# Kernel tuning notes

Hardware: AMD Instinct MI355X
Metric: run time of the kernel (lower is better)

The kernel has to match this reference:

```python
import jax, jax.numpy as jnp
import numpy as np
import math

S, B, H, NH = 2048, 2, 2048, 16
HN = H // NH  # head dim = 128

def setup_inputs() -> dict:
    key = jax.random.key(0)
    ks = jax.random.split(key, 5)
    hidden_states = jax.random.normal(ks[0], (S, B, H), dtype=jnp.float32)
    # causal mask: True means masked (filled with -10000), broadcast over heads
    attention_mask = jnp.triu(jnp.ones((S, S), dtype=bool), k=1)[None, None].repeat(B, axis=0)
    w_qkv = jax.random.normal(ks[1], (3 * H, H), dtype=jnp.float32) * (1.0 / math.sqrt(H))
    b_qkv = jax.random.normal(ks[2], (3 * H,), dtype=jnp.float32) * 0.02
    w_dense = jax.random.normal(ks[3], (H, H), dtype=jnp.float32) * (1.0 / math.sqrt(H))
    b_dense = jax.random.normal(ks[4], (H,), dtype=jnp.float32) * 0.02
    return {"hidden_states": hidden_states, "attention_mask": attention_mask,
            "w_qkv": w_qkv, "b_qkv": b_qkv, "w_dense": w_dense, "b_dense": b_dense}

def reference(hidden_states, attention_mask, w_qkv, b_qkv, w_dense, b_dense):
    s, b, h = hidden_states.shape
    nh, hn = NH, h // NH
    # QKV projection (ColumnParallelLinear, world_size=1)
    qkv = hidden_states @ w_qkv.T + b_qkv                # [s, b, 3h]
    qkv = qkv.reshape(s, b, nh, 3 * hn)
    q, k, v = jnp.split(qkv, 3, axis=-1)                 # each [s, b, nh, hn]
    q = q.transpose(1, 2, 0, 3)                          # [b, nh, s, hn]
    k = k.transpose(1, 2, 0, 3)
    v = v.transpose(1, 2, 0, 3)
    # norm_factor = sqrt(hn)*coeff, softmax rescales by coeff -> net 1/sqrt(hn)
    scores = jnp.einsum('bnqh,bnkh->bnqk', q, k) / jnp.float32(math.sqrt(hn))
    scores = jnp.where(attention_mask, jnp.float32(-10000.0), scores)
    probs = jax.nn.softmax(scores, axis=-1)              # [b, nh, s, s]
    ctx = jnp.einsum('bnqk,bnkh->bnqh', probs, v)        # [b, nh, s, hn]
    ctx = ctx.transpose(2, 0, 1, 3).reshape(s, b, h)     # [s, b, h]
    # RowParallelLinear with skip_bias_add=True: bias returned separately
    output = ctx @ w_dense.T
    return output, b_dense
```

## Files before the change

kernel.cpp:

```cpp
#include <hip/hip_runtime.h>

typedef unsigned short u16;
typedef unsigned int   u32;
typedef __attribute__((ext_vector_type(8))) short bf16x8;
typedef __attribute__((ext_vector_type(4))) float f32x4;

#define S_LEN 2048
#define B_SZ  2
#define H_DIM 2048
#define NH_   16
#define HN_   128
#define M_TOK 4096
#define NQKV  6144
#define NT_   (S_LEN / 64)

__device__ __forceinline__ u16 f2bf(float f) {
    u32 x = __float_as_uint(f);
    return (u16)((x + 0x7fffu + ((x >> 16) & 1u)) >> 16);
}

__device__ __forceinline__ void async16(const void* g, void* l) {
    __builtin_amdgcn_global_load_lds((const __attribute__((address_space(1))) void*)g,
                                     (__attribute__((address_space(3))) void*)l,
                                     16, 0, 0);
}

__global__ __launch_bounds__(256) void cvt3(
    const float* __restrict__ a, u16* __restrict__ oa, int na,
    const float* __restrict__ b, u16* __restrict__ ob, int nb,
    const float* __restrict__ c, u16* __restrict__ oc, int nc)
{
    int g = blockIdx.x * 256 + threadIdx.x;
    const float* in; u16* out; int idx;
    if (g < na)           { in = a; out = oa; idx = g; }
    else if (g < na + nb) { in = b; out = ob; idx = g - na; }
    else if (g < na + nb + nc) { in = c; out = oc; idx = g - na - nb; }
    else return;
    int i = idx * 4;
    float4 v = *(const float4*)&in[i];
    ushort4 o;
    o.x = f2bf(v.x); o.y = f2bf(v.y); o.z = f2bf(v.z); o.w = f2bf(v.w);
    *(ushort4*)&out[i] = o;
}

template<int EPI>
__global__ __launch_bounds__(256) void gemm_mfma(
    const u16* __restrict__ A, const u16* __restrict__ W,
    const float* __restrict__ bias, float* __restrict__ Cout,
    u16* __restrict__ Qb, u16* __restrict__ Kb, u16* __restrict__ Vt,
    int M, int N, int K)
{
    __shared__ __align__(16) u16 Af[2][8 * 64 * 8];
    __shared__ __align__(16) u16 Bf[2][8 * 64 * 8];
    const int t = threadIdx.x, l = t & 63, w = t >> 6;
    const int quad = l >> 4, ln = l & 15;
    const int wm = w >> 1, wn = w & 1;
    const int m0 = blockIdx.y * 128, n0 = blockIdx.x * 128;

    f32x4 acc[4][4];
#pragma unroll
    for (int i = 0; i < 4; ++i)
#pragma unroll
        for (int j = 0; j < 4; ++j)
#pragma unroll
            for (int r = 0; r < 4; ++r) acc[i][j][r] = 0.f;

    auto stage = [&](int buf, int k0) {
#pragma unroll
        for (int i = 0; i < 2; ++i) {
            int mb = i * 4 + w;
            async16(&A[(size_t)(m0 + mb * 16 + ln) * K + k0 + quad * 8],
                    &Af[buf][(mb * 64 + l) * 8]);
            async16(&W[(size_t)(n0 + mb * 16 + ln) * K + k0 + quad * 8],
                    &Bf[buf][(mb * 64 + l) * 8]);
        }
    };

    stage(0, 0);
    __syncthreads();

    const int NIT = K / 32;
#pragma unroll 1
    for (int kk = 0; kk < NIT; ++kk) {
        const int cur = kk & 1;
        if (kk + 1 < NIT) stage(cur ^ 1, (kk + 1) * 32);

        bf16x8 af[4], bfr[4];
#pragma unroll
        for (int x = 0; x < 4; ++x) {
            af[x]  = *(const bf16x8*)&Af[cur][((wm * 4 + x) * 64 + l) * 8];
            bfr[x] = *(const bf16x8*)&Bf[cur][((wn * 4 + x) * 64 + l) * 8];
        }
#pragma unroll
        for (int mt = 0; mt < 4; ++mt)
#pragma unroll
            for (int nt = 0; nt < 4; ++nt)
                acc[mt][nt] = __builtin_amdgcn_mfma_f32_16x16x32_bf16(
                    af[mt], bfr[nt], acc[mt][nt], 0, 0, 0);
        __syncthreads();
    }

    if constexpr (EPI == 0) {
#pragma unroll
        for (int mt = 0; mt < 4; ++mt)
#pragma unroll
            for (int nt = 0; nt < 4; ++nt) {
                int col = n0 + (wn * 4 + nt) * 16 + ln;
#pragma unroll
                for (int r = 0; r < 4; ++r) {
                    int row = m0 + wm * 64 + mt * 16 + quad * 4 + r;
                    Cout[(size_t)row * N + col] = acc[mt][nt][r];
                }
            }
    } else {
        const float kQS = 0.08838834764831845f * 1.44269504088896340f;
#pragma unroll
        for (int nt = 0; nt < 4; ++nt) {
            int col  = n0 + (wn * 4 + nt) * 16 + ln;
            int head = col / 384;
            int g    = col - head * 384;
            int sec  = g >> 7;
            int d    = g & 127;
            float bv = bias[col];
#pragma unroll
            for (int mt = 0; mt < 4; ++mt)
#pragma unroll
                for (int r = 0; r < 4; ++r) {
                    int tok = m0 + wm * 64 + mt * 16 + quad * 4 + r;
                    int s = tok >> 1, bb = tok & 1;
                    float v = acc[mt][nt][r] + bv;
                    if (sec == 0)
                        Qb[((size_t)(bb * NH_ + head) * S_LEN + s) * HN_ + d] = f2bf(v * kQS);
                    else if (sec == 1)
                        Kb[((size_t)(bb * NH_ + head) * S_LEN + s) * HN_ + d] = f2bf(v);
                    else
                        Vt[((size_t)(bb * NH_ + head) * HN_ + d) * S_LEN + s] = f2bf(v);
                }
        }
    }
}

__global__ __launch_bounds__(256) void attn_mfma(
    const u16* __restrict__ Qb, const u16* __restrict__ Kb,
    const u16* __restrict__ Vt, u16* __restrict__ Ctx)
{
    __shared__ __align__(16) u16 Ks[2][16 * 64 * 8];
    __shared__ __align__(16) u16 Vs[2][16 * 64 * 8];
    __shared__ __align__(16) u16 Psm[4][16][72];

    const int t = threadIdx.x, l = t & 63, w = t >> 6;
    const int quad = l >> 4, ln = l & 15;
    const int j = blockIdx.x;
    const int n = blockIdx.y, b = blockIdx.z;
    const u16* Qh = Qb + (size_t)(b * NH_ + n) * S_LEN * HN_;
    const u16* Kh = Kb + (size_t)(b * NH_ + n) * S_LEN * HN_;
    const u16* Vh = Vt + (size_t)(b * NH_ + n) * HN_ * S_LEN;

#pragma unroll 1
    for (int phase = 0; phase < 2; ++phase) {
        const int qt = phase ? j : (NT_ - 1 - j);
        const int q0 = qt * 64;

#pragma unroll
        for (int i = 0; i < 4; ++i)
            async16(&Qh[(size_t)(q0 + i * 16 + ln) * HN_ + w * 32 + quad * 8],
                    &Ks[1][((i * 4 + w) * 64 + l) * 8]);
#pragma unroll
        for (int i = 0; i < 4; ++i) {
            async16(&Kh[(size_t)(i * 16 + ln) * HN_ + w * 32 + quad * 8],
                    &Ks[0][((i * 4 + w) * 64 + l) * 8]);
            int dv = i * 4 + w, dt = dv >> 1, ks = dv & 1;
            async16(&Vh[(size_t)(dt * 16 + ln) * S_LEN + ks * 32 + quad * 8],
                    &Vs[0][(dv * 64 + l) * 8]);
        }
        __syncthreads();

        bf16x8 qf[4];
#pragma unroll
        for (int ks = 0; ks < 4; ++ks)
            qf[ks] = *(const bf16x8*)&Ks[1][((w * 4 + ks) * 64 + l) * 8];
        __syncthreads();

        float m_i[4], l_i[4];
        f32x4 acco[8];
#pragma unroll
        for (int r = 0; r < 4; ++r) { m_i[r] = -1e30f; l_i[r] = 0.f; }
#pragma unroll
        for (int dt = 0; dt < 8; ++dt)
#pragma unroll
            for (int r = 0; r < 4; ++r) acco[dt][r] = 0.f;

#pragma unroll 1
        for (int kt = 0; kt <= qt; ++kt) {
            const int cur = kt & 1;

            if (kt < qt) {
                const int nxt = cur ^ 1;
#pragma unroll
                for (int i = 0; i < 4; ++i) {
                    async16(&Kh[(size_t)((kt + 1) * 64 + i * 16 + ln) * HN_ + w * 32 + quad * 8],
                            &Ks[nxt][((i * 4 + w) * 64 + l) * 8]);
                    int dv = i * 4 + w, dt = dv >> 1, ks = dv & 1;
                    async16(&Vh[(size_t)(dt * 16 + ln) * S_LEN + (kt + 1) * 64 + ks * 32 + quad * 8],
                            &Vs[nxt][(dv * 64 + l) * 8]);
                }
            }

            f32x4 sc[4];
#pragma unroll
            for (int nt = 0; nt < 4; ++nt)
#pragma unroll
                for (int r = 0; r < 4; ++r) sc[nt][r] = 0.f;
#pragma unroll
            for (int nt = 0; nt < 4; ++nt)
#pragma unroll
                for (int ks = 0; ks < 4; ++ks) {
                    bf16x8 kf = *(const bf16x8*)&Ks[cur][((nt * 4 + ks) * 64 + l) * 8];
                    sc[nt] = __builtin_amdgcn_mfma_f32_16x16x32_bf16(qf[ks], kf, sc[nt], 0, 0, 0);
                }

            if (kt == qt) {
#pragma unroll
                for (int nt = 0; nt < 4; ++nt)
#pragma unroll
                    for (int r = 0; r < 4; ++r)
                        if (nt * 16 + ln > w * 16 + quad * 4 + r) sc[nt][r] = -1e30f;
            }

            float corr[4];
#pragma unroll
            for (int r = 0; r < 4; ++r) {
                float mx = fmaxf(fmaxf(sc[0][r], sc[1][r]), fmaxf(sc[2][r], sc[3][r]));
                mx = fmaxf(mx, __shfl_xor(mx, 1));
                mx = fmaxf(mx, __shfl_xor(mx, 2));
                mx = fmaxf(mx, __shfl_xor(mx, 4));
                mx = fmaxf(mx, __shfl_xor(mx, 8));
                float mnew = fmaxf(m_i[r], mx);
                corr[r] = exp2f(m_i[r] - mnew);
                m_i[r] = mnew;
            }
#pragma unroll
            for (int r = 0; r < 4; ++r) {
                float ps = 0.f;
#pragma unroll
                for (int nt = 0; nt < 4; ++nt) {
                    float p = exp2f(sc[nt][r] - m_i[r]);
                    ps += p;
                    Psm[w][quad * 4 + r][nt * 16 + ln] = f2bf(p);
                }
                l_i[r] = l_i[r] * corr[r] + ps;
            }

#pragma unroll
            for (int dt = 0; dt < 8; ++dt)
#pragma unroll
                for (int r = 0; r < 4; ++r) acco[dt][r] *= corr[r];

            bf16x8 pf[2];
#pragma unroll
            for (int ks = 0; ks < 2; ++ks)
                pf[ks] = *(const bf16x8*)&Psm[w][ln][ks * 32 + quad * 8];
#pragma unroll
            for (int dt = 0; dt < 8; ++dt)
#pragma unroll
                for (int ks = 0; ks < 2; ++ks) {
                    bf16x8 vf = *(const bf16x8*)&Vs[cur][((dt * 2 + ks) * 64 + l) * 8];
                    acco[dt] = __builtin_amdgcn_mfma_f32_16x16x32_bf16(pf[ks], vf, acco[dt], 0, 0, 0);
                }
            __syncthreads();
        }

#pragma unroll
        for (int r = 0; r < 4; ++r) {
            float s = l_i[r];
            s += __shfl_xor(s, 1);
            s += __shfl_xor(s, 2);
            s += __shfl_xor(s, 4);
            s += __shfl_xor(s, 8);
            l_i[r] = 1.f / s;
        }
#pragma unroll
        for (int dt = 0; dt < 8; ++dt)
#pragma unroll
            for (int r = 0; r < 4; ++r) {
                int srow = q0 + w * 16 + quad * 4 + r;
                Ctx[((size_t)(srow * B_SZ + b)) * H_DIM + n * HN_ + dt * 16 + ln] =
                    f2bf(acco[dt][r] * l_i[r]);
            }
    }
}

__global__ void copy_bias(const float* __restrict__ b_dense, float* __restrict__ out)
{
    int t = blockIdx.x * 256 + threadIdx.x;
    if (t < H_DIM) out[(size_t)M_TOK * H_DIM + t] = b_dense[t];
}

extern "C" void kernel_launch(void* const* d_in, const int* in_sizes, int n_in,
                              void* d_out, int out_size, void* d_ws, size_t ws_size,
                              hipStream_t stream)
{
    const float* hs      = (const float*)d_in[0];
    const float* w_qkv   = (const float*)d_in[2];
    const float* b_qkv   = (const float*)d_in[3];
    const float* w_dense = (const float*)d_in[4];
    const float* b_dense = (const float*)d_in[5];
    float* out = (float*)d_out;

    u16* hs_bf = (u16*)d_ws;
    u16* wq_bf = hs_bf + (size_t)M_TOK * H_DIM;
    u16* wd_bf = wq_bf + (size_t)NQKV * H_DIM;
    u16* Qb    = wd_bf + (size_t)H_DIM * H_DIM;
    u16* Kb    = Qb    + (size_t)M_TOK * H_DIM;
    u16* Vt    = Kb    + (size_t)M_TOK * H_DIM;
    u16* Ctx   = Vt    + (size_t)M_TOK * H_DIM;

    const int g1 = (M_TOK * H_DIM) / 4;
    const int g2 = (NQKV * H_DIM) / 4;
    const int g3 = (H_DIM * H_DIM) / 4;
    cvt3<<<(g1 + g2 + g3 + 255) / 256, 256, 0, stream>>>(
        hs, hs_bf, g1, w_qkv, wq_bf, g2, w_dense, wd_bf, g3);

    gemm_mfma<1><<<dim3(NQKV / 128, M_TOK / 128), 256, 0, stream>>>(
        hs_bf, wq_bf, b_qkv, nullptr, Qb, Kb, Vt, M_TOK, NQKV, H_DIM);

    attn_mfma<<<dim3(NT_ / 2, NH_, B_SZ), 256, 0, stream>>>(Qb, Kb, Vt, Ctx);

    gemm_mfma<0><<<dim3(H_DIM / 128, M_TOK / 128), 256, 0, stream>>>(
        Ctx, wd_bf, nullptr, out, nullptr, nullptr, nullptr, M_TOK, H_DIM, H_DIM);

    copy_bias<<<(H_DIM + 255) / 256, 256, 0, stream>>>(b_dense, out);
}
```

Measured before the change: 507.3 us.

## Use a producer warp with a 4-stage LDS ring in the GEMMs

Both GEMM kernels now run a dedicated producer wavefront that issues async global-to-LDS loads into a 4-deep ring buffer. The four compute wavefronts synchronise with it through ready/done counters in shared memory instead of a block-wide barrier on every K step. The aim is to hide load latency and let compute waves avoid full barriers. In exchange the block grows to 320 threads, LDS use doubles, spin-waits are added, and correctness depends on hand-written waitcnt encodings.

```diff
diff --git a/kernel.cpp b/kernel.cpp
--- a/kernel.cpp
+++ b/kernel.cpp
@@ -44,19 +44,59 @@
 }
 
 template<int EPI>
-__global__ __launch_bounds__(256) void gemm_mfma(
+__global__ __launch_bounds__(320) void gemm_pc(
     const u16* __restrict__ A, const u16* __restrict__ W,
     const float* __restrict__ bias, float* __restrict__ Cout,
     u16* __restrict__ Qb, u16* __restrict__ Kb, u16* __restrict__ Vt,
     int M, int N, int K)
 {
-    __shared__ __align__(16) u16 Af[2][8 * 64 * 8];
-    __shared__ __align__(16) u16 Bf[2][8 * 64 * 8];
+    __shared__ __align__(16) u16 Aring[4][8 * 64 * 8];
+    __shared__ __align__(16) u16 Bring[4][8 * 64 * 8];
+    __shared__ u32 ready[4], done[4];
+
     const int t = threadIdx.x, l = t & 63, w = t >> 6;
     const int quad = l >> 4, ln = l & 15;
+    const int m0 = blockIdx.y * 128, n0 = blockIdx.x * 128;
+    const int NIT = K / 32;
+
+    if (t < 4) { ready[t] = 0; done[t] = 0; }
+    __syncthreads();
+
+    if (w == 4) {
+#pragma unroll 1
+        for (int kk = 0; kk < NIT; ++kk) {
+            const int s = kk & 3;
+            if (kk >= 4) {
+                const u32 need = 4u * (u32)(kk >> 2);
+                while (__hip_atomic_load(&done[s], __ATOMIC_ACQUIRE,
+                                         __HIP_MEMORY_SCOPE_WORKGROUP) < need)
+                    __builtin_amdgcn_s_sleep(2);
+            }
+            const int k0 = kk * 32;
+#pragma unroll
+            for (int mb = 0; mb < 8; ++mb)
+                async16(&A[(size_t)(m0 + mb * 16 + ln) * K + k0 + quad * 8],
+                        &Aring[s][(mb * 64 + l) * 8]);
+#pragma unroll
+            for (int mb = 0; mb < 8; ++mb)
+                async16(&W[(size_t)(n0 + mb * 16 + ln) * K + k0 + quad * 8],
+                        &Bring[s][(mb * 64 + l) * 8]);
+            if (kk >= 2) {
+                __builtin_amdgcn_s_waitcnt(0x8F70);
+                __hip_atomic_store(&ready[(kk - 2) & 3], (u32)((kk - 2) >> 2) + 1u,
+                                   __ATOMIC_RELEASE, __HIP_MEMORY_SCOPE_WORKGROUP);
+            }
+        }
+        __builtin_amdgcn_s_waitcnt(0x4F70);
+        __hip_atomic_store(&ready[(NIT - 2) & 3], (u32)((NIT - 2) >> 2) + 1u,
+                           __ATOMIC_RELEASE, __HIP_MEMORY_SCOPE_WORKGROUP);
+        __builtin_amdgcn_s_waitcnt(0x0F70);
+        __hip_atomic_store(&ready[(NIT - 1) & 3], (u32)((NIT - 1) >> 2) + 1u,
+                           __ATOMIC_RELEASE, __HIP_MEMORY_SCOPE_WORKGROUP);
+        return;
+    }
+
     const int wm = w >> 1, wn = w & 1;
-    const int m0 = blockIdx.y * 128, n0 = blockIdx.x * 128;
-
     f32x4 acc[4][4];
 #pragma unroll
     for (int i = 0; i < 4; ++i)
@@ -65,31 +105,19 @@
 #pragma unroll
             for (int r = 0; r < 4; ++r) acc[i][j][r] = 0.f;
 
-    auto stage = [&](int buf, int k0) {
-#pragma unroll
-        for (int i = 0; i < 2; ++i) {
-            int mb = i * 4 + w;
-            async16(&A[(size_t)(m0 + mb * 16 + ln) * K + k0 + quad * 8],
-                    &Af[buf][(mb * 64 + l) * 8]);
-            async16(&W[(size_t)(n0 + mb * 16 + ln) * K + k0 + quad * 8],
-                    &Bf[buf][(mb * 64 + l) * 8]);
-        }
-    };
-
-    stage(0, 0);
-    __syncthreads();
-
-    const int NIT = K / 32;
 #pragma unroll 1
     for (int kk = 0; kk < NIT; ++kk) {
-        const int cur = kk & 1;
-        if (kk + 1 < NIT) stage(cur ^ 1, (kk + 1) * 32);
+        const int s = kk & 3;
+        const u32 tag = (u32)(kk >> 2) + 1u;
+        while (__hip_atomic_load(&ready[s], __ATOMIC_ACQUIRE,
+                                 __HIP_MEMORY_SCOPE_WORKGROUP) < tag)
+            __builtin_amdgcn_s_sleep(2);
 
         bf16x8 af[4], bfr[4];
 #pragma unroll
         for (int x = 0; x < 4; ++x) {
-            af[x]  = *(const bf16x8*)&Af[cur][((wm * 4 + x) * 64 + l) * 8];
-            bfr[x] = *(const bf16x8*)&Bf[cur][((wn * 4 + x) * 64 + l) * 8];
+            af[x]  = *(const bf16x8*)&Aring[s][((wm * 4 + x) * 64 + l) * 8];
+            bfr[x] = *(const bf16x8*)&Bring[s][((wn * 4 + x) * 64 + l) * 8];
         }
 #pragma unroll
         for (int mt = 0; mt < 4; ++mt)
@@ -97,7 +125,9 @@
             for (int nt = 0; nt < 4; ++nt)
                 acc[mt][nt] = __builtin_amdgcn_mfma_f32_16x16x32_bf16(
                     af[mt], bfr[nt], acc[mt][nt], 0, 0, 0);
-        __syncthreads();
+
+        __hip_atomic_fetch_add(&done[s], 1u, __ATOMIC_RELEASE,
+                               __HIP_MEMORY_SCOPE_WORKGROUP);
     }
 
     if constexpr (EPI == 0) {
@@ -321,12 +351,12 @@
     cvt3<<<(g1 + g2 + g3 + 255) / 256, 256, 0, stream>>>(
         hs, hs_bf, g1, w_qkv, wq_bf, g2, w_dense, wd_bf, g3);
 
-    gemm_mfma<1><<<dim3(NQKV / 128, M_TOK / 128), 256, 0, stream>>>(
+    gemm_pc<1><<<dim3(NQKV / 128, M_TOK / 128), 320, 0, stream>>>(
         hs_bf, wq_bf, b_qkv, nullptr, Qb, Kb, Vt, M_TOK, NQKV, H_DIM);
 
     attn_mfma<<<dim3(NT_ / 2, NH_, B_SZ), 256, 0, stream>>>(Qb, Kb, Vt, Ctx);
 
-    gemm_mfma<0><<<dim3(H_DIM / 128, M_TOK / 128), 256, 0, stream>>>(
+    gemm_pc<0><<<dim3(H_DIM / 128, M_TOK / 128), 320, 0, stream>>>(
         Ctx, wd_bf, nullptr, out, nullptr, nullptr, nullptr, M_TOK, H_DIM, H_DIM);
 
     copy_bias<<<(H_DIM + 255) / 256, 256, 0, stream>>>(b_dense, out);
```

New measurement: 619.8 us. 1.22x slower.

## Replace async global-to-LDS loads with register-staged double-buffered GEMM pipeline

Applied to the files above, without the earlier changes.

The GEMM mainloop now loads tiles from global memory into registers two steps ahead, then stores them to LDS after computing on the current buffer. It replaces the direct global_load_lds path and full __syncthreads with an lgkmcnt wait plus s_barrier, and unrolls the loop by two across alternating register sets. The goal is to hide global load latency behind MFMA work and to cut barrier overhead. In exchange it uses more VGPRs and adds explicit LDS stores.

```diff
diff --git a/kernel.cpp b/kernel.cpp
--- a/kernel.cpp
+++ b/kernel.cpp
@@ -13,6 +13,9 @@
 #define M_TOK 4096
 #define NQKV  6144
 #define NT_   (S_LEN / 64)
+
+#define LGKM_BARRIER asm volatile("s_waitcnt lgkmcnt(0)\n\ts_barrier" ::: "memory")
+#define SCHED_FENCE  asm volatile("" ::: "memory")
 
 __device__ __forceinline__ u16 f2bf(float f) {
     u32 x = __float_as_uint(f);
@@ -44,7 +47,7 @@
 }
 
 template<int EPI>
-__global__ __launch_bounds__(256) void gemm_mfma(
+__global__ __launch_bounds__(256) void gemm_rs(
     const u16* __restrict__ A, const u16* __restrict__ W,
     const float* __restrict__ bias, float* __restrict__ Cout,
     u16* __restrict__ Qb, u16* __restrict__ Kb, u16* __restrict__ Vt,
@@ -57,6 +60,12 @@
     const int wm = w >> 1, wn = w & 1;
     const int m0 = blockIdx.y * 128, n0 = blockIdx.x * 128;
 
+    const int c0 = t, c1 = t + 256;
+    const u16* pa0 = &A[(size_t)(m0 + (c0 >> 6) * 16 + (c0 & 15)) * K + ((c0 >> 4) & 3) * 8];
+    const u16* pa1 = &A[(size_t)(m0 + (c1 >> 6) * 16 + (c1 & 15)) * K + ((c1 >> 4) & 3) * 8];
+    const u16* pb0 = &W[(size_t)(n0 + (c0 >> 6) * 16 + (c0 & 15)) * K + ((c0 >> 4) & 3) * 8];
+    const u16* pb1 = &W[(size_t)(n0 + (c1 >> 6) * 16 + (c1 & 15)) * K + ((c1 >> 4) & 3) * 8];
+
     f32x4 acc[4][4];
 #pragma unroll
     for (int i = 0; i < 4; ++i)
@@ -65,40 +74,63 @@
 #pragma unroll
             for (int r = 0; r < 4; ++r) acc[i][j][r] = 0.f;
 
-    auto stage = [&](int buf, int k0) {
-#pragma unroll
-        for (int i = 0; i < 2; ++i) {
-            int mb = i * 4 + w;
-            async16(&A[(size_t)(m0 + mb * 16 + ln) * K + k0 + quad * 8],
-                    &Af[buf][(mb * 64 + l) * 8]);
-            async16(&W[(size_t)(n0 + mb * 16 + ln) * K + k0 + quad * 8],
-                    &Bf[buf][(mb * 64 + l) * 8]);
-        }
-    };
-
-    stage(0, 0);
-    __syncthreads();
+    bf16x8 xa0, xa1, xb0, xb1;
+    bf16x8 ya0, ya1, yb0, yb1;
+
+#define LD_TILE(k0, a0, a1, b0, b1)                 \
+    do {                                            \
+        a0 = *(const bf16x8*)(pa0 + (k0));          \
+        a1 = *(const bf16x8*)(pa1 + (k0));          \
+        b0 = *(const bf16x8*)(pb0 + (k0));          \
+        b1 = *(const bf16x8*)(pb1 + (k0));          \
+        SCHED_FENCE;                                \
+    } while (0)
+
+#define ST_TILE(buf, a0, a1, b0, b1)                \
+    do {                                            \
+        *(bf16x8*)&Af[buf][t * 8]        = a0;      \
+        *(bf16x8*)&Af[buf][t * 8 + 2048] = a1;      \
+        *(bf16x8*)&Bf[buf][t * 8]        = b0;      \
+        *(bf16x8*)&Bf[buf][t * 8 + 2048] = b1;      \
+    } while (0)
+
+#define COMPUTE(buf)                                                          \
+    do {                                                                      \
+        bf16x8 af[4], bfr[4];                                                 \
+        _Pragma("unroll")                                                     \
+        for (int x = 0; x < 4; ++x) {                                         \
+            af[x]  = *(const bf16x8*)&Af[buf][((wm * 4 + x) * 64 + l) * 8];   \
+            bfr[x] = *(const bf16x8*)&Bf[buf][((wn * 4 + x) * 64 + l) * 8];   \
+        }                                                                     \
+        _Pragma("unroll")                                                     \
+        for (int mt = 0; mt < 4; ++mt)                                        \
+            _Pragma("unroll")                                                 \
+            for (int nt = 0; nt < 4; ++nt)                                    \
+                acc[mt][nt] = __builtin_amdgcn_mfma_f32_16x16x32_bf16(        \
+                    af[mt], bfr[nt], acc[mt][nt], 0, 0, 0);                   \
+    } while (0)
 
     const int NIT = K / 32;
+
+    LD_TILE(0, xa0, xa1, xb0, xb1);
+    ST_TILE(0, xa0, xa1, xb0, xb1);
+    LD_TILE(32, ya0, ya1, yb0, yb1);
+    LGKM_BARRIER;
+
 #pragma unroll 1
-    for (int kk = 0; kk < NIT; ++kk) {
-        const int cur = kk & 1;
-        if (kk + 1 < NIT) stage(cur ^ 1, (kk + 1) * 32);
-
-        bf16x8 af[4], bfr[4];
-#pragma unroll
-        for (int x = 0; x < 4; ++x) {
-            af[x]  = *(const bf16x8*)&Af[cur][((wm * 4 + x) * 64 + l) * 8];
-            bfr[x] = *(const bf16x8*)&Bf[cur][((wn * 4 + x) * 64 + l) * 8];
-        }
-#pragma unroll
-        for (int mt = 0; mt < 4; ++mt)
-#pragma unroll
-            for (int nt = 0; nt < 4; ++nt)
-                acc[mt][nt] = __builtin_amdgcn_mfma_f32_16x16x32_bf16(
-                    af[mt], bfr[nt], acc[mt][nt], 0, 0, 0);
-        __syncthreads();
+    for (int kk = 0; kk < NIT; kk += 2) {
+        if (kk + 2 < NIT) LD_TILE((kk + 2) * 32, xa0, xa1, xb0, xb1);
+        COMPUTE(0);
+        ST_TILE(1, ya0, ya1, yb0, yb1);
+        LGKM_BARRIER;
+        if (kk + 3 < NIT) LD_TILE((kk + 3) * 32, ya0, ya1, yb0, yb1);
+        COMPUTE(1);
+        if (kk + 2 < NIT) ST_TILE(0, xa0, xa1, xb0, xb1);
+        LGKM_BARRIER;
     }
+#undef LD_TILE
+#undef ST_TILE
+#undef COMPUTE
 
     if constexpr (EPI == 0) {
 #pragma unroll
@@ -321,12 +353,12 @@
     cvt3<<<(g1 + g2 + g3 + 255) / 256, 256, 0, stream>>>(
         hs, hs_bf, g1, w_qkv, wq_bf, g2, w_dense, wd_bf, g3);
 
-    gemm_mfma<1><<<dim3(NQKV / 128, M_TOK / 128), 256, 0, stream>>>(
+    gemm_rs<1><<<dim3(NQKV / 128, M_TOK / 128), 256, 0, stream>>>(
         hs_bf, wq_bf, b_qkv, nullptr, Qb, Kb, Vt, M_TOK, NQKV, H_DIM);
 
     attn_mfma<<<dim3(NT_ / 2, NH_, B_SZ), 256, 0, stream>>>(Qb, Kb, Vt, Ctx);
 
-    gemm_mfma<0><<<dim3(H_DIM / 128, M_TOK / 128), 256, 0, stream>>>(
+    gemm_rs<0><<<dim3(H_DIM / 128, M_TOK / 128), 256, 0, stream>>>(
         Ctx, wd_bf, nullptr, out, nullptr, nullptr, nullptr, M_TOK, H_DIM, H_DIM);
 
     copy_bias<<<(H_DIM + 255) / 256, 256, 0, stream>>>(b_dense, out);
```

After: 502.4 us. About the same (-1.0%).
